# Optimization experiments

Hardware: AMD Instinct MI355X
Metric: run time of the kernel (lower is better)

Reference implementation:

```python
import jax, jax.numpy as jnp
import numpy as np


def setup_inputs() -> dict:
    key = jax.random.key(0)
    k1, k2, k3, k4 = jax.random.split(key, 4)
    B, N, M, D = 32, 512, 512, 1024
    return {
        "x1": jax.random.normal(k1, (B, N, D), dtype=jnp.float32),
        "x2": jax.random.normal(k2, (B, M, D), dtype=jnp.float32),
        "mask1": jax.random.randint(k3, (B, N), 0, 2, dtype=jnp.int32),
        "mask2": jax.random.randint(k4, (B, M), 0, 2, dtype=jnp.int32),
    }


def _masked_attention(x, align, mask):
    # align: [B, Q, K], mask: [B, K] (broadcast over Q, matching tf.tile over seq_len)
    neg_inf = jnp.asarray(-jnp.inf, dtype=align.dtype)
    align = jnp.where(mask[:, None, :] == 0, neg_inf, align)
    attn = jax.nn.softmax(align, axis=-1)  # [B, Q, K]
    return jnp.matmul(attn, x)  # [B, Q, D]


def reference(x1, x2, mask1, mask2):
    # align12[b, n, m] = x1[b, n, :] . x2[b, m, :]
    align12 = jnp.einsum("bnd,bmd->bnm", x1, x2)
    align21 = jnp.transpose(align12, (0, 2, 1))
    x1_coef = _masked_attention(x2, align12, mask2)  # [B, N, D]
    x2_coef = _masked_attention(x1, align21, mask1)  # [B, M, D]
    return (x1_coef, x2_coef)
```

## Files before the change

kernel.cpp:

```cpp
#include <hip/hip_runtime.h>
#include <hip/hip_bf16.h>

#define BB 32
#define NN 512
#define MM 512
#define DD 1024

typedef __attribute__((ext_vector_type(8))) short short8;
typedef __attribute__((ext_vector_type(4))) float f32x4;

#define ASYNC_COPY16(g, l) \
    __builtin_amdgcn_global_load_lds((__attribute__((address_space(1))) void*)(g), \
                                     (__attribute__((address_space(3))) void*)(l), 16, 0, 0)

__device__ inline unsigned short f2bf(float f) {
    unsigned int u = __float_as_uint(f);
    u += 0x7fffu + ((u >> 16) & 1u);
    return (unsigned short)(u >> 16);
}

#define SPLIT1(vv, hh, ll) { unsigned short h_ = f2bf(vv); \
    float hf_ = __uint_as_float((unsigned int)h_ << 16); \
    hh = h_; ll = f2bf((vv) - hf_); }

__global__ __launch_bounds__(256) void convert_split_t(
    const float* __restrict__ x1, const float* __restrict__ x2,
    unsigned short* __restrict__ x1h, unsigned short* __restrict__ x1l,
    unsigned short* __restrict__ x1hT,
    unsigned short* __restrict__ x2h, unsigned short* __restrict__ x2l,
    unsigned short* __restrict__ x2hT) {
    int bid = blockIdx.x;
    const float* src; unsigned short *h, *l, *hT;
    if (bid < 2048) { src = x1; h = x1h; l = x1l; hT = x1hT; }
    else            { src = x2; h = x2h; l = x2l; hT = x2hT; bid -= 2048; }
    int b = bid >> 6; int rem = bid & 63;
    int r0 = (rem >> 4) * 128, c0 = (rem & 15) * 64;
    __shared__ unsigned short T[64 * 130];
    int t = threadIdx.x;
    int i = t >> 4, j4 = (t & 15) * 4;
    ushort4 HH[8], LL[8];
#pragma unroll
    for (int p = 0; p < 8; ++p) {
        int r = i + p * 16;
        size_t off = ((size_t)b * 512 + r0 + r) * 1024 + c0 + j4;
        float4 v = *(const float4*)&src[off];
        ushort4 hh, ll;
        SPLIT1(v.x, hh.x, ll.x) SPLIT1(v.y, hh.y, ll.y)
        SPLIT1(v.z, hh.z, ll.z) SPLIT1(v.w, hh.w, ll.w)
        HH[p] = hh; LL[p] = ll;
        T[(j4 + 0) * 130 + r] = hh.x;
        T[(j4 + 1) * 130 + r] = hh.y;
        T[(j4 + 2) * 130 + r] = hh.z;
        T[(j4 + 3) * 130 + r] = hh.w;
    }
    __syncthreads();
#pragma unroll
    for (int p = 0; p < 8; ++p) {
        int r = i + p * 16;
        size_t off = ((size_t)b * 512 + r0 + r) * 1024 + c0 + j4;
        *(ushort4*)&h[off] = HH[p];
        *(ushort4*)&l[off] = LL[p];
    }
    int rr = (t & 31) * 4;
    int cb = t >> 5;
#pragma unroll
    for (int pp = 0; pp < 8; ++pp) {
        int c = cb + pp * 8;
        uint2 o;
        o.x = *(const unsigned int*)&T[c * 130 + rr];
        o.y = *(const unsigned int*)&T[c * 130 + rr + 2];
        *(uint2*)&hT[((size_t)b * 1024 + c0 + c) * 512 + r0 + rr] = o;
    }
}

__global__ __launch_bounds__(512, 4) void gemm_align(
    const unsigned short* __restrict__ x1h, const unsigned short* __restrict__ x1l,
    const unsigned short* __restrict__ x2h, const unsigned short* __restrict__ x2l,
    const int* __restrict__ mask1, const int* __restrict__ mask2,
    float* __restrict__ alg,
    float* __restrict__ rp_max, float* __restrict__ rp_sum,
    float* __restrict__ cp_max, float* __restrict__ cp_sum) {
    __shared__ unsigned short S[2][16384];
    int bid = blockIdx.x;
    int nb = (bid & 7) * 64 + (bid >> 3);
    int b = nb >> 4; int tl = nb & 15;
    int nt = tl >> 2, mt = tl & 3;
    int n0 = nt * 128, m0 = mt * 128;
    int t = threadIdx.x; int w = t >> 6; int l = t & 63;
    int lane16 = l & 15, q = l >> 4, q8 = q * 8;
    int wr = (w >> 2) * 64;
    int wc = (w & 3) * 32;
    f32x4 acc[4][2];
#pragma unroll
    for (int i = 0; i < 4; ++i)
#pragma unroll
        for (int j = 0; j < 2; ++j) acc[i][j] = (f32x4){0.f, 0.f, 0.f, 0.f};
    const unsigned short* gs[4];
    int ls[4];
#pragma unroll
    for (int s = 0; s < 4; ++s) {
        int qq = w * 4 + s;
        int row0 = (qq & 7) * 16;
        const unsigned short* base; int lb;
        if (qq < 8)       { base = x1h + ((size_t)b * 512 + n0) * 1024; lb = 0; }
        else if (qq < 16) { base = x1l + ((size_t)b * 512 + n0) * 1024; lb = 4096; }
        else if (qq < 24) { base = x2h + ((size_t)b * 512 + m0) * 1024; lb = 8192; }
        else              { base = x2l + ((size_t)b * 512 + m0) * 1024; lb = 12288; }
        gs[s] = base + (size_t)(row0 + (l >> 2)) * 1024 + (l & 3) * 8;
        ls[s] = lb + row0 * 32 + l * 8;
    }
#pragma unroll
    for (int s = 0; s < 4; ++s)
        ASYNC_COPY16(gs[s], &S[0][ls[s]]);
    __syncthreads();
    int cur = 0;
    for (int kk = 0; kk < 1024; kk += 32) {
        if (kk + 32 < 1024) {
#pragma unroll
            for (int s = 0; s < 4; ++s)
                ASYNC_COPY16(gs[s] + kk + 32, &S[cur ^ 1][ls[s]]);
        }
        const unsigned short* Sb = S[cur];
        short8 ah[4], al[4], bh[2], bl[2];
#pragma unroll
        for (int i = 0; i < 4; ++i) {
            int off = (wr + i * 16 + lane16) * 32 + q8;
            ah[i] = *(const short8*)&Sb[off];
            al[i] = *(const short8*)&Sb[4096 + off];
        }
#pragma unroll
        for (int j = 0; j < 2; ++j) {
            int off = (wc + j * 16 + lane16) * 32 + q8;
            bh[j] = *(const short8*)&Sb[8192 + off];
            bl[j] = *(const short8*)&Sb[12288 + off];
        }
#pragma unroll
        for (int i = 0; i < 4; ++i)
#pragma unroll
            for (int j = 0; j < 2; ++j) {
                acc[i][j] = __builtin_amdgcn_mfma_f32_16x16x32_bf16(ah[i], bh[j], acc[i][j], 0, 0, 0);
                acc[i][j] = __builtin_amdgcn_mfma_f32_16x16x32_bf16(ah[i], bl[j], acc[i][j], 0, 0, 0);
                acc[i][j] = __builtin_amdgcn_mfma_f32_16x16x32_bf16(al[i], bh[j], acc[i][j], 0, 0, 0);
            }
        __syncthreads();
        cur ^= 1;
    }
    float* ob = alg + ((size_t)b * 512 + n0 + wr) * 512 + m0 + wc;
    int q4 = q * 4;
#pragma unroll
    for (int i = 0; i < 4; ++i)
#pragma unroll
        for (int j = 0; j < 2; ++j)
#pragma unroll
            for (int r = 0; r < 4; ++r)
                ob[(size_t)(i * 16 + q4 + r) * 512 + j * 16 + lane16] = acc[i][j][r];
    int mk2[2];
#pragma unroll
    for (int j = 0; j < 2; ++j) mk2[j] = mask2[b * 512 + m0 + wc + j * 16 + lane16];
    int mk1r[4][4];
#pragma unroll
    for (int i = 0; i < 4; ++i)
#pragma unroll
        for (int r = 0; r < 4; ++r) mk1r[i][r] = mask1[b * 512 + n0 + wr + i * 16 + q4 + r];
#pragma unroll
    for (int j = 0; j < 2; ++j) {
        float cm = -3.0e38f;
#pragma unroll
        for (int i = 0; i < 4; ++i)
#pragma unroll
            for (int r = 0; r < 4; ++r)
                if (mk1r[i][r]) cm = fmaxf(cm, acc[i][j][r]);
        cm = fmaxf(cm, __shfl_xor(cm, 16));
        cm = fmaxf(cm, __shfl_xor(cm, 32));
        float cs = 0.f;
#pragma unroll
        for (int i = 0; i < 4; ++i)
#pragma unroll
            for (int r = 0; r < 4; ++r)
                cs += mk1r[i][r] ? __expf(acc[i][j][r] - cm) : 0.f;
        cs += __shfl_xor(cs, 16);
        cs += __shfl_xor(cs, 32);
        if (q == 0) {
            size_t o = ((size_t)b * 8 + nt * 2 + (w >> 2)) * 512 + m0 + wc + j * 16 + lane16;
            cp_max[o] = cm;
            cp_sum[o] = cs;
        }
    }
    float* rmS = (float*)&S[0][0];
    float* rsS = rmS + 512;
#pragma unroll
    for (int i = 0; i < 4; ++i)
#pragma unroll
        for (int r = 0; r < 4; ++r) {
            float v0 = acc[i][0][r], v1 = acc[i][1][r];
            float rm = fmaxf(mk2[0] ? v0 : -3.0e38f, mk2[1] ? v1 : -3.0e38f);
            rm = fmaxf(rm, __shfl_xor(rm, 1));
            rm = fmaxf(rm, __shfl_xor(rm, 2));
            rm = fmaxf(rm, __shfl_xor(rm, 4));
            rm = fmaxf(rm, __shfl_xor(rm, 8));
            float rs = (mk2[0] ? __expf(v0 - rm) : 0.f) + (mk2[1] ? __expf(v1 - rm) : 0.f);
            rs += __shfl_xor(rs, 1);
            rs += __shfl_xor(rs, 2);
            rs += __shfl_xor(rs, 4);
            rs += __shfl_xor(rs, 8);
            if (lane16 == 0) {
                int row = i * 16 + q4 + r;
                rmS[w * 64 + row] = rm;
                rsS[w * 64 + row] = rs;
            }
        }
    __syncthreads();
    if (t < 128) {
        int grp = t >> 6, rloc = t & 63;
        float M = -3.0e38f;
#pragma unroll
        for (int ww = 0; ww < 4; ++ww) M = fmaxf(M, rmS[(grp * 4 + ww) * 64 + rloc]);
        float Ssum = 0.f;
#pragma unroll
        for (int ww = 0; ww < 4; ++ww)
            Ssum += rsS[(grp * 4 + ww) * 64 + rloc] * __expf(rmS[(grp * 4 + ww) * 64 + rloc] - M);
        size_t o = ((size_t)b * 4 + mt) * 512 + n0 + t;
        rp_max[o] = M;
        rp_sum[o] = Ssum;
    }
}

__global__ __launch_bounds__(256) void combine_stats(
    const float* __restrict__ rp_max, const float* __restrict__ rp_sum,
    const float* __restrict__ cp_max, const float* __restrict__ cp_sum,
    float* __restrict__ rowmax, float* __restrict__ rowinv,
    float* __restrict__ colmax, float* __restrict__ colinv) {
    int idx = blockIdx.x * 256 + threadIdx.x;
    if (idx < 16384) {
        int b = idx >> 9, n = idx & 511;
        float M = -3.0e38f;
#pragma unroll
        for (int tt = 0; tt < 4; ++tt) M = fmaxf(M, rp_max[((size_t)b * 4 + tt) * 512 + n]);
        float S = 0.f;
#pragma unroll
        for (int tt = 0; tt < 4; ++tt) {
            size_t o = ((size_t)b * 4 + tt) * 512 + n;
            S += rp_sum[o] * __expf(rp_max[o] - M);
        }
        rowmax[idx] = M;
        rowinv[idx] = 1.0f / S;
    } else {
        int id2 = idx - 16384;
        int b = id2 >> 9, m = id2 & 511;
        float M = -3.0e38f;
#pragma unroll
        for (int tt = 0; tt < 8; ++tt) M = fmaxf(M, cp_max[((size_t)b * 8 + tt) * 512 + m]);
        float S = 0.f;
#pragma unroll
        for (int tt = 0; tt < 8; ++tt) {
            size_t o = ((size_t)b * 8 + tt) * 512 + m;
            S += cp_sum[o] * __expf(cp_max[o] - M);
        }
        colmax[id2] = M;
        colinv[id2] = 1.0f / S;
    }
}

__global__ __launch_bounds__(256) void apply_softmax(
    const float* __restrict__ alg, const int* __restrict__ mask1,
    const int* __restrict__ mask2,
    const float* __restrict__ rowmax, const float* __restrict__ rowinv,
    const float* __restrict__ colmax, const float* __restrict__ colinv,
    unsigned short* __restrict__ attn12, unsigned short* __restrict__ attn21) {
    int bid = blockIdx.x; int b = bid >> 6; int rem = bid & 63;
    int m0 = (rem >> 3) * 64, n0 = (rem & 7) * 64;
    int t = threadIdx.x;
    __shared__ float lds[64 * 65];
    int jj = t & 63; int ii = t >> 6;
    int mk2 = mask2[b * 512 + m0 + jj];
    unsigned short e12[16];
#pragma unroll
    for (int p = 0; p < 16; ++p) {
        int n = ii + p * 4;
        float v = alg[((size_t)b * 512 + n0 + n) * 512 + m0 + jj];
        lds[n * 65 + jj] = v;
        float rm = rowmax[b * 512 + n0 + n];
        float ri = rowinv[b * 512 + n0 + n];
        e12[p] = mk2 ? f2bf(__expf(v - rm) * ri) : (unsigned short)0;
    }
    __syncthreads();
#pragma unroll
    for (int p = 0; p < 16; ++p) {
        int n = ii + p * 4;
        attn12[((size_t)b * 512 + n0 + n) * 512 + m0 + jj] = e12[p];
    }
    int mk1 = mask1[b * 512 + n0 + jj];
#pragma unroll
    for (int p = 0; p < 16; ++p) {
        int mm = ii + p * 4;
        float cm = colmax[b * 512 + m0 + mm];
        float ci = colinv[b * 512 + m0 + mm];
        float v = lds[jj * 65 + mm];
        unsigned short pv = mk1 ? f2bf(__expf(v - cm) * ci) : (unsigned short)0;
        attn21[((size_t)b * 512 + m0 + mm) * 512 + n0 + jj] = pv;
    }
}

__global__ __launch_bounds__(256) void gemm_pv(
    const unsigned short* __restrict__ P, const unsigned short* __restrict__ VT,
    float* __restrict__ out) {
    __shared__ unsigned short S[2][2][4096];
    int bid = blockIdx.x;
    int nb = (bid & 7) * 128 + (bid >> 3);
    int b = nb >> 5; int rem = nb & 31;
    int n0 = (rem >> 3) * 128, d0 = (rem & 7) * 128;
    int t = threadIdx.x; int w = t >> 6; int l = t & 63;
    int lane16 = l & 15, q8 = (l >> 4) * 8;
    int wr = (w >> 1) * 64, wc = (w & 1) * 64;
    f32x4 acc[4][4];
#pragma unroll
    for (int i = 0; i < 4; ++i)
#pragma unroll
        for (int j = 0; j < 4; ++j) acc[i][j] = (f32x4){0.f, 0.f, 0.f, 0.f};
    const unsigned short* gA = P + ((size_t)b * 512 + n0) * 512;
    const unsigned short* gB = VT + ((size_t)b * DD + d0) * 512;
    int w2 = w & 1;
    int side = (w < 2) ? 0 : 1;
    const unsigned short* gp = (w < 2) ? gA : gB;
    const unsigned short* gbase = gp + (size_t)(w2 * 64 + (l >> 2)) * 512 + (l & 3) * 8;
    int lofs = w2 * 2048;
#pragma unroll
    for (int p = 0; p < 4; ++p)
        ASYNC_COPY16(gbase + (size_t)(p * 16) * 512, &S[0][side][lofs + p * 512]);
    __syncthreads();
    int cur = 0;
    for (int kk = 0; kk < 512; kk += 32) {
        if (kk + 32 < 512) {
#pragma unroll
            for (int p = 0; p < 4; ++p)
                ASYNC_COPY16(gbase + (size_t)(p * 16) * 512 + kk + 32,
                             &S[cur ^ 1][side][lofs + p * 512]);
        }
        short8 af[4], bf[4];
#pragma unroll
        for (int i = 0; i < 4; ++i)
            af[i] = *(const short8*)&S[cur][0][(wr + i * 16 + lane16) * 32 + q8];
#pragma unroll
        for (int j = 0; j < 4; ++j)
            bf[j] = *(const short8*)&S[cur][1][(wc + j * 16 + lane16) * 32 + q8];
#pragma unroll
        for (int i = 0; i < 4; ++i)
#pragma unroll
            for (int j = 0; j < 4; ++j)
                acc[i][j] = __builtin_amdgcn_mfma_f32_16x16x32_bf16(af[i], bf[j], acc[i][j], 0, 0, 0);
        __syncthreads();
        cur ^= 1;
    }
    int q4 = (l >> 4) * 4;
#pragma unroll
    for (int i = 0; i < 4; ++i)
#pragma unroll
        for (int j = 0; j < 4; ++j)
#pragma unroll
            for (int r = 0; r < 4; ++r) {
                int rr = n0 + wr + i * 16 + q4 + r;
                int dd = d0 + wc + j * 16 + lane16;
                out[((size_t)b * 512 + rr) * DD + dd] = acc[i][j][r];
            }
}

extern "C" void kernel_launch(void* const* d_in, const int* in_sizes, int n_in,
                              void* d_out, int out_size, void* d_ws, size_t ws_size,
                              hipStream_t stream) {
    const float* x1 = (const float*)d_in[0];
    const float* x2 = (const float*)d_in[1];
    const int* mask1 = (const int*)d_in[2];
    const int* mask2 = (const int*)d_in[3];
    char* ws = (char*)d_ws;
    unsigned short* x1h  = (unsigned short*)(ws);
    unsigned short* x2h  = (unsigned short*)(ws + 33554432UL);
    unsigned short* x1hT = (unsigned short*)(ws + 67108864UL);
    unsigned short* x2hT = (unsigned short*)(ws + 100663296UL);
    unsigned short* x1l  = (unsigned short*)(ws + 134217728UL);
    unsigned short* x2l  = (unsigned short*)(ws + 167772160UL);
    float* alg           = (float*)(ws + 201326592UL);
    unsigned short* attn12 = (unsigned short*)(ws + 134217728UL);
    float* rowmax        = (float*)(ws + 150994944UL);
    float* rowinv        = (float*)(ws + 151060480UL);
    float* colmax        = (float*)(ws + 151126016UL);
    float* colinv        = (float*)(ws + 151191552UL);
    unsigned short* attn21 = (unsigned short*)(ws + 167772160UL);
    float* out1 = (float*)d_out;
    float* out2 = out1 + (size_t)BB * NN * DD;
    float* rp_max = (float*)d_out;
    float* rp_sum = rp_max + 65536;
    float* cp_max = rp_sum + 65536;
    float* cp_sum = cp_max + 131072;

    convert_split_t<<<4096, 256, 0, stream>>>(x1, x2, x1h, x1l, x1hT, x2h, x2l, x2hT);
    gemm_align<<<512, 512, 0, stream>>>(x1h, x1l, x2h, x2l, mask1, mask2, alg,
                                        rp_max, rp_sum, cp_max, cp_sum);
    combine_stats<<<128, 256, 0, stream>>>(rp_max, rp_sum, cp_max, cp_sum,
                                           rowmax, rowinv, colmax, colinv);
    apply_softmax<<<2048, 256, 0, stream>>>(alg, mask1, mask2, rowmax, rowinv,
                                            colmax, colinv, attn12, attn21);
    gemm_pv<<<1024, 256, 0, stream>>>(attn12, x2hT, out1);
    gemm_pv<<<1024, 256, 0, stream>>>(attn21, x1hT, out2);
}
```

Before: 422.5 us.

## Drop transposed bf16 copies and transpose V inside the PV GEMM via LDS

```diff
diff --git a/kernel.cpp b/kernel.cpp
--- a/kernel.cpp
+++ b/kernel.cpp
@@ -23,53 +23,26 @@
     float hf_ = __uint_as_float((unsigned int)h_ << 16); \
     hh = h_; ll = f2bf((vv) - hf_); }
 
-__global__ __launch_bounds__(256) void convert_split_t(
+__global__ __launch_bounds__(256) void convert_split(
     const float* __restrict__ x1, const float* __restrict__ x2,
     unsigned short* __restrict__ x1h, unsigned short* __restrict__ x1l,
-    unsigned short* __restrict__ x1hT,
-    unsigned short* __restrict__ x2h, unsigned short* __restrict__ x2l,
-    unsigned short* __restrict__ x2hT) {
-    int bid = blockIdx.x;
-    const float* src; unsigned short *h, *l, *hT;
-    if (bid < 2048) { src = x1; h = x1h; l = x1l; hT = x1hT; }
-    else            { src = x2; h = x2h; l = x2l; hT = x2hT; bid -= 2048; }
-    int b = bid >> 6; int rem = bid & 63;
-    int r0 = (rem >> 4) * 128, c0 = (rem & 15) * 64;
-    __shared__ unsigned short T[64 * 130];
-    int t = threadIdx.x;
-    int i = t >> 4, j4 = (t & 15) * 4;
-    ushort4 HH[8], LL[8];
-#pragma unroll
-    for (int p = 0; p < 8; ++p) {
-        int r = i + p * 16;
-        size_t off = ((size_t)b * 512 + r0 + r) * 1024 + c0 + j4;
-        float4 v = *(const float4*)&src[off];
+    unsigned short* __restrict__ x2h, unsigned short* __restrict__ x2l) {
+    size_t g = (size_t)blockIdx.x * 256 + threadIdx.x;
+#pragma unroll
+    for (int r = 0; r < 2; ++r) {
+        size_t idx = g + (size_t)r * 2097152;
+        float4 v = ((const float4*)x1)[idx];
         ushort4 hh, ll;
         SPLIT1(v.x, hh.x, ll.x) SPLIT1(v.y, hh.y, ll.y)
         SPLIT1(v.z, hh.z, ll.z) SPLIT1(v.w, hh.w, ll.w)
-        HH[p] = hh; LL[p] = ll;
-        T[(j4 + 0) * 130 + r] = hh.x;
-        T[(j4 + 1) * 130 + r] = hh.y;
-        T[(j4 + 2) * 130 + r] = hh.z;
-        T[(j4 + 3) * 130 + r] = hh.w;
-    }
-    __syncthreads();
-#pragma unroll
-    for (int p = 0; p < 8; ++p) {
-        int r = i + p * 16;
-        size_t off = ((size_t)b * 512 + r0 + r) * 1024 + c0 + j4;
-        *(ushort4*)&h[off] = HH[p];
-        *(ushort4*)&l[off] = LL[p];
-    }
-    int rr = (t & 31) * 4;
-    int cb = t >> 5;
-#pragma unroll
-    for (int pp = 0; pp < 8; ++pp) {
-        int c = cb + pp * 8;
-        uint2 o;
-        o.x = *(const unsigned int*)&T[c * 130 + rr];
-        o.y = *(const unsigned int*)&T[c * 130 + rr + 2];
-        *(uint2*)&hT[((size_t)b * 1024 + c0 + c) * 512 + r0 + rr] = o;
+        ((ushort4*)x1h)[idx] = hh;
+        ((ushort4*)x1l)[idx] = ll;
+        float4 u = ((const float4*)x2)[idx];
+        ushort4 hh2, ll2;
+        SPLIT1(u.x, hh2.x, ll2.x) SPLIT1(u.y, hh2.y, ll2.y)
+        SPLIT1(u.z, hh2.z, ll2.z) SPLIT1(u.w, hh2.w, ll2.w)
+        ((ushort4*)x2h)[idx] = hh2;
+        ((ushort4*)x2l)[idx] = ll2;
     }
 }
 
@@ -302,15 +275,16 @@
 }
 
 __global__ __launch_bounds__(256) void gemm_pv(
-    const unsigned short* __restrict__ P, const unsigned short* __restrict__ VT,
+    const unsigned short* __restrict__ P, const unsigned short* __restrict__ V,
     float* __restrict__ out) {
-    __shared__ unsigned short S[2][2][4096];
+    __shared__ unsigned short SA[2][4096];
+    __shared__ unsigned int   SB[2][32 * 65];
     int bid = blockIdx.x;
     int nb = (bid & 7) * 128 + (bid >> 3);
     int b = nb >> 5; int rem = nb & 31;
     int n0 = (rem >> 3) * 128, d0 = (rem & 7) * 128;
     int t = threadIdx.x; int w = t >> 6; int l = t & 63;
-    int lane16 = l & 15, q8 = (l >> 4) * 8;
+    int lane16 = l & 15, q = l >> 4, q8 = q * 8;
     int wr = (w >> 1) * 64, wc = (w & 1) * 64;
     f32x4 acc[4][4];
 #pragma unroll
@@ -318,40 +292,72 @@
 #pragma unroll
         for (int j = 0; j < 4; ++j) acc[i][j] = (f32x4){0.f, 0.f, 0.f, 0.f};
     const unsigned short* gA = P + ((size_t)b * 512 + n0) * 512;
-    const unsigned short* gB = VT + ((size_t)b * DD + d0) * 512;
-    int w2 = w & 1;
-    int side = (w < 2) ? 0 : 1;
-    const unsigned short* gp = (w < 2) ? gA : gB;
-    const unsigned short* gbase = gp + (size_t)(w2 * 64 + (l >> 2)) * 512 + (l & 3) * 8;
-    int lofs = w2 * 2048;
-#pragma unroll
-    for (int p = 0; p < 4; ++p)
-        ASYNC_COPY16(gbase + (size_t)(p * 16) * 512, &S[0][side][lofs + p * 512]);
+    const unsigned short* gsA[2];
+    int ldsa[2];
+#pragma unroll
+    for (int s = 0; s < 2; ++s) {
+        int a = w * 2 + s;
+        gsA[s] = gA + (size_t)(a * 16 + (l >> 2)) * 512 + (l & 3) * 8;
+        ldsa[s] = a * 512 + l * 8;
+    }
+    int dch = l & 15;
+    int mloc[2]; mloc[0] = w * 4 + q; mloc[1] = mloc[0] + 16;
+    const unsigned short* gB0[2];
+#pragma unroll
+    for (int s = 0; s < 2; ++s)
+        gB0[s] = V + (size_t)b * 524288 + (size_t)mloc[s] * 1024 + d0 + dch * 8;
+    union U8 { short8 s; unsigned int u[4]; };
+    U8 bv[2];
+#pragma unroll
+    for (int s = 0; s < 2; ++s) bv[s].s = *(const short8*)gB0[s];
+#pragma unroll
+    for (int s = 0; s < 2; ++s)
+        ASYNC_COPY16(gsA[s], &SA[0][ldsa[s]]);
+#pragma unroll
+    for (int s = 0; s < 2; ++s)
+#pragma unroll
+        for (int c = 0; c < 4; ++c)
+            SB[0][mloc[s] * 65 + dch * 4 + c] = bv[s].u[c];
     __syncthreads();
     int cur = 0;
     for (int kk = 0; kk < 512; kk += 32) {
-        if (kk + 32 < 512) {
-#pragma unroll
-            for (int p = 0; p < 4; ++p)
-                ASYNC_COPY16(gbase + (size_t)(p * 16) * 512 + kk + 32,
-                             &S[cur ^ 1][side][lofs + p * 512]);
-        }
-        short8 af[4], bf[4];
+        int more = (kk + 32 < 512);
+        if (more) {
+#pragma unroll
+            for (int s = 0; s < 2; ++s) bv[s].s = *(const short8*)(gB0[s] + (size_t)(kk + 32) * 1024);
+#pragma unroll
+            for (int s = 0; s < 2; ++s)
+                ASYNC_COPY16(gsA[s] + kk + 32, &SA[cur ^ 1][ldsa[s]]);
+        }
+        short8 af[4];
 #pragma unroll
         for (int i = 0; i < 4; ++i)
-            af[i] = *(const short8*)&S[cur][0][(wr + i * 16 + lane16) * 32 + q8];
-#pragma unroll
-        for (int j = 0; j < 4; ++j)
-            bf[j] = *(const short8*)&S[cur][1][(wc + j * 16 + lane16) * 32 + q8];
+            af[i] = *(const short8*)&SA[cur][(wr + i * 16 + lane16) * 32 + q8];
+        const unsigned short* Bs = (const unsigned short*)SB[cur];
+        short8 bf[4];
+#pragma unroll
+        for (int j = 0; j < 4; ++j) {
+            int col = wc + j * 16 + lane16;
+#pragma unroll
+            for (int e = 0; e < 8; ++e)
+                bf[j][e] = (short)Bs[(q8 + e) * 130 + col];
+        }
 #pragma unroll
         for (int i = 0; i < 4; ++i)
 #pragma unroll
             for (int j = 0; j < 4; ++j)
                 acc[i][j] = __builtin_amdgcn_mfma_f32_16x16x32_bf16(af[i], bf[j], acc[i][j], 0, 0, 0);
+        if (more) {
+#pragma unroll
+            for (int s = 0; s < 2; ++s)
+#pragma unroll
+                for (int c = 0; c < 4; ++c)
+                    SB[cur ^ 1][mloc[s] * 65 + dch * 4 + c] = bv[s].u[c];
+        }
         __syncthreads();
         cur ^= 1;
     }
-    int q4 = (l >> 4) * 4;
+    int q4 = q * 4;
 #pragma unroll
     for (int i = 0; i < 4; ++i)
 #pragma unroll
@@ -374,8 +380,6 @@
     char* ws = (char*)d_ws;
     unsigned short* x1h  = (unsigned short*)(ws);
     unsigned short* x2h  = (unsigned short*)(ws + 33554432UL);
-    unsigned short* x1hT = (unsigned short*)(ws + 67108864UL);
-    unsigned short* x2hT = (unsigned short*)(ws + 100663296UL);
     unsigned short* x1l  = (unsigned short*)(ws + 134217728UL);
     unsigned short* x2l  = (unsigned short*)(ws + 167772160UL);
     float* alg           = (float*)(ws + 201326592UL);
@@ -392,13 +396,13 @@
     float* cp_max = rp_sum + 65536;
     float* cp_sum = cp_max + 131072;
 
-    convert_split_t<<<4096, 256, 0, stream>>>(x1, x2, x1h, x1l, x1hT, x2h, x2l, x2hT);
+    convert_split<<<8192, 256, 0, stream>>>(x1, x2, x1h, x1l, x2h, x2l);
     gemm_align<<<512, 512, 0, stream>>>(x1h, x1l, x2h, x2l, mask1, mask2, alg,
                                         rp_max, rp_sum, cp_max, cp_sum);
     combine_stats<<<128, 256, 0, stream>>>(rp_max, rp_sum, cp_max, cp_sum,
                                            rowmax, rowinv, colmax, colinv);
     apply_softmax<<<2048, 256, 0, stream>>>(alg, mask1, mask2, rowmax, rowinv,
                                             colmax, colinv, attn12, attn21);
-    gemm_pv<<<1024, 256, 0, stream>>>(attn12, x2hT, out1);
-    gemm_pv<<<1024, 256, 0, stream>>>(attn21, x1hT, out2);
-}
+    gemm_pv<<<1024, 256, 0, stream>>>(attn12, x2h, out1);
+    gemm_pv<<<1024, 256, 0, stream>>>(attn21, x1h, out2);
+}
```

Measured after the change: 408.7 us. -3.3%, faster.
